# Optimization experiments

Measured on AMD Instinct MI355X. Metric: run time of the kernel, lower is better.

Reference implementation:

```python
import jax, jax.numpy as jnp
import numpy as np

V, E, H, K, B, T = 50000, 256, 256, 32, 64, 512


def _lstm_dir(x, w_ih, w_hh, b, reverse):
    # x: [B,T,D] -> [B,T,H]; torch gate order i,f,g,o; b = b_ih + b_hh combined
    xg = jnp.einsum('btd,gd->btg', x, w_ih) + b          # [B,T,4H]
    xs = jnp.swapaxes(xg, 0, 1)                          # [T,B,4H]
    if reverse:
        xs = xs[::-1]
    Hh = w_hh.shape[1]
    init = (jnp.zeros((x.shape[0], Hh), x.dtype), jnp.zeros((x.shape[0], Hh), x.dtype))

    def step(carry, g_t):
        h, c = carry
        g = g_t + h @ w_hh.T
        i, f, gg, o = jnp.split(g, 4, axis=-1)
        c = jax.nn.sigmoid(f) * c + jax.nn.sigmoid(i) * jnp.tanh(gg)
        h = jax.nn.sigmoid(o) * jnp.tanh(c)
        return (h, c), h

    _, hs = jax.lax.scan(step, init, xs)
    if reverse:
        hs = hs[::-1]
    return jnp.swapaxes(hs, 0, 1)


def _bilstm(x, params):
    out = x
    for (wif, whf, bf, wib, whb, bb) in params:  # inter-layer dropout = identity (eval)
        f = _lstm_dir(out, wif, whf, bf, False)
        bwd = _lstm_dir(out, wib, whb, bb, True)
        out = jnp.concatenate([f, bwd], axis=-1)
    return out


def _crf_loss(em, labels, crf_start, crf_end, crf_trans):
    # numerator (mask is all ones -> every timestep counts)
    num = crf_start[labels[:, 0]] + crf_end[labels[:, -1]]
    num = num + jnp.take_along_axis(em, labels[:, :, None], 2)[..., 0].sum(1)
    num = num + crf_trans[labels[:, :-1], labels[:, 1:]].sum(1)
    # log-partition via forward algorithm
    def pstep(alpha, em_t):
        return jax.nn.logsumexp(alpha[:, :, None] + crf_trans[None], axis=1) + em_t, None

    alpha0 = crf_start[None] + em[:, 0]
    alpha, _ = jax.lax.scan(pstep, alpha0, jnp.swapaxes(em[:, 1:], 0, 1))
    logZ = jax.nn.logsumexp(alpha + crf_end[None], axis=-1)
    # loss = -crf(emissions, labels, mask) with reduction='sum'
    return -(num - logZ).sum()


def _viterbi(em, crf_start, crf_end, crf_trans):
    score0 = crf_start[None] + em[:, 0]

    def vstep(score, em_t):
        ns = score[:, :, None] + crf_trans[None]         # [B,K,K]
        bp = jnp.argmax(ns, axis=1)                      # [B,K]
        return jnp.max(ns, axis=1) + em_t, bp

    score, bps = jax.lax.scan(vstep, score0, jnp.swapaxes(em[:, 1:], 0, 1))
    last = jnp.argmax(score + crf_end[None], axis=-1)    # [B]

    def back(tag, bp):
        prev = jnp.take_along_axis(bp, tag[:, None], axis=1)[:, 0]
        return prev, prev

    _, prevs = jax.lax.scan(back, last, bps[::-1])
    tags = jnp.concatenate([prevs[::-1], last[None]], axis=0)  # [T,B]
    return jnp.swapaxes(tags, 0, 1)


def setup_inputs():
    key = jax.random.key(0)
    ks = iter(jax.random.split(key, 32))
    s = 0.05
    d = {}
    d["input_ids"] = jax.random.randint(next(ks), (B, T), 0, V)
    d["labels"] = jax.random.randint(next(ks), (B, T), 0, K)
    d["mask"] = jnp.ones((B, T), jnp.int32)
    d["emb_table"] = jax.random.normal(next(ks), (V, E)) * s
    for l, din in ((0, E), (1, 2 * H)):
        for dr in ("f", "b"):
            d[f"w_ih_{l}{dr}"] = jax.random.normal(next(ks), (4 * H, din)) * s
            d[f"w_hh_{l}{dr}"] = jax.random.normal(next(ks), (4 * H, H)) * s
            d[f"b_{l}{dr}"] = jax.random.normal(next(ks), (4 * H,)) * s
    d["w_out"] = jax.random.normal(next(ks), (K, 2 * H)) * s
    d["b_out"] = jnp.zeros((K,))
    d["crf_start"] = jax.random.normal(next(ks), (K,)) * s
    d["crf_end"] = jax.random.normal(next(ks), (K,)) * s
    d["crf_trans"] = jax.random.normal(next(ks), (K, K)) * s
    return d


def reference(input_ids, labels, mask, emb_table, w_ih_0f, w_hh_0f, b_0f, w_ih_0b, w_hh_0b, b_0b, w_ih_1f, w_hh_1f, b_1f, w_ih_1b, w_hh_1b, b_1b, w_out, b_out, crf_start, crf_end, crf_trans):
    emb = emb_table[input_ids]  # dropout = identity (eval mode)
    # mask is all ones -> sort/pack/unsort in the original is an identity permutation
    params = [(w_ih_0f, w_hh_0f, b_0f, w_ih_0b, w_hh_0b, b_0b),
              (w_ih_1f, w_hh_1f, b_1f, w_ih_1b, w_hh_1b, b_1b)]
    out = _bilstm(emb, params)                           # [B,T,2H]
    em = jnp.einsum('bth,kh->btk', out, w_out) + b_out   # emissions [B,T,K]
    loss = _crf_loss(em, labels, crf_start, crf_end, crf_trans)
    preds = _viterbi(em, crf_start, crf_end, crf_trans)
    return (loss, preds)
```

## Files before the change

kernel.cpp:

```cpp
#include <hip/hip_runtime.h>
#include <math.h>


constexpr int TLEN = 512, CS = 64, NCH = 8;

constexpr size_t N_OUT  = (size_t)TLEN * 64 * 512;
constexpr size_t O_OUT0 = 0;
constexpr size_t O_OUT1 = N_OUT;
constexpr size_t O_XG   = 2 * N_OUT;
constexpr size_t N_XG   = (size_t)2 * CS * 64 * 1024;
constexpr size_t O_EM   = O_XG;
constexpr size_t O_WQ   = O_XG + N_XG;
constexpr size_t N_WQ   = (size_t)2 * 256 * 256 * 4;
constexpr size_t O_CST  = O_WQ + N_WQ;
constexpr size_t N_CST  = (size_t)2 * 2 * 64 * 256;
constexpr size_t WS_FLOATS = O_CST + N_CST;

__global__ void initz(float* dout) { if (threadIdx.x == 0) dout[0] = 0.f; }

__global__ void ws_too_small_k(float* dout, int n) {
  int i = blockIdx.x * 256 + threadIdx.x;
  if (i < n) dout[i] = 1e30f;
}

__global__ __launch_bounds__(256)
void prep_w(const float* __restrict__ whhf, const float* __restrict__ whhb,
            float* __restrict__ wq) {
  const int k = blockIdx.x & 255, d = blockIdx.x >> 8, u = threadIdx.x;
  const float* W = d ? whhb : whhf;
  float4 v;
  v.x = W[(size_t)(0   + u) * 256 + k];
  v.y = W[(size_t)(256 + u) * 256 + k];
  v.z = W[(size_t)(512 + u) * 256 + k];
  v.w = W[(size_t)(768 + u) * 256 + k];
  reinterpret_cast<float4*>(wq)[(size_t)d * 65536 + k * 256 + u] = v;
}

template <int KTOT, int BN, int MODE>
__global__ __launch_bounds__(256)
void gemm_k(const float* __restrict__ A, const int* __restrict__ ids,
            const float* __restrict__ Wf, const float* __restrict__ Wb,
            const float* __restrict__ bf, const float* __restrict__ bb,
            float* __restrict__ C, int s0) {
  constexpr int BK = 16;
  constexpr int NC = (BN == 128) ? 8 : 2;
  __shared__ float As[BK][132];
  __shared__ float Bs[BK][BN + 4];
  const int tid = threadIdx.x;
  const int m0 = blockIdx.x * 128, n0 = blockIdx.y * BN, d = blockIdx.z;
  const float* W = (MODE < 2 && d) ? Wb : Wf;
  const float* bias = (MODE < 2 && d) ? bb : bf;
  const int mg = tid & 15, ng = tid >> 4;
  const int rb = tid >> 2;
  const int kq = (tid & 3) << 2;

  int arow[2];
  #pragma unroll
  for (int p = 0; p < 2; ++p) {
    if (MODE == 2) {
      arow[p] = m0 + p * 64 + rb;
    } else {
      int s = s0 + (m0 >> 6) + p;
      int t = d ? (TLEN - 1 - s) : s;
      arow[p] = (MODE == 0) ? ids[rb * TLEN + t] : (t * 64 + rb);
    }
  }

  float acc[8][NC];
  #pragma unroll
  for (int i = 0; i < 8; ++i)
    #pragma unroll
    for (int jj = 0; jj < NC; ++jj) acc[i][jj] = 0.f;

  for (int kt = 0; kt < KTOT; kt += BK) {
    #pragma unroll
    for (int p = 0; p < 2; ++p) {
      float4 v = *reinterpret_cast<const float4*>(A + (size_t)arow[p] * KTOT + kt + kq);
      int r = p * 64 + rb;
      As[kq + 0][r] = v.x; As[kq + 1][r] = v.y;
      As[kq + 2][r] = v.z; As[kq + 3][r] = v.w;
    }
    #pragma unroll
    for (int p = 0; p < 2; ++p) {
      int r = p * 64 + rb;
      if (BN == 128 || (p == 0 && rb < BN)) {
        float4 v = *reinterpret_cast<const float4*>(W + (size_t)(n0 + r) * KTOT + kt + kq);
        Bs[kq + 0][r] = v.x; Bs[kq + 1][r] = v.y;
        Bs[kq + 2][r] = v.z; Bs[kq + 3][r] = v.w;
      }
    }
    __syncthreads();
    #pragma unroll
    for (int k = 0; k < BK; ++k) {
      float a[8];
      #pragma unroll
      for (int i = 0; i < 8; ++i) a[i] = As[k][i * 16 + mg];
      if (BN == 128) {
        float w[8];
        float4 w0 = *reinterpret_cast<const float4*>(&Bs[k][ng * 8]);
        float4 w1 = *reinterpret_cast<const float4*>(&Bs[k][ng * 8 + 4]);
        w[0] = w0.x; w[1] = w0.y; w[2] = w0.z; w[3] = w0.w;
        w[4] = w1.x; w[5] = w1.y; w[6] = w1.z; w[7] = w1.w;
        #pragma unroll
        for (int i = 0; i < 8; ++i)
          #pragma unroll
          for (int jj = 0; jj < 8; ++jj) acc[i][jj] += a[i] * w[jj];
      } else {
        float w0 = Bs[k][ng * 2], w1 = Bs[k][ng * 2 + 1];
        #pragma unroll
        for (int i = 0; i < 8; ++i) {
          acc[i][0] += a[i] * w0;
          acc[i][1] += a[i] * w1;
        }
      }
    }
    __syncthreads();
  }

  if (BN == 128) {
    float bv[8];
    #pragma unroll
    for (int jj = 0; jj < 8; ++jj) bv[jj] = bias[n0 + ng * 8 + jj];
    #pragma unroll
    for (int i = 0; i < 8; ++i) {
      const int ml = i * 16 + mg;
      float* cp = C + ((size_t)d * 4096 + m0 + ml) * 1024 + n0 + ng * 8;
      float4 o0, o1;
      o0.x = acc[i][0] + bv[0]; o0.y = acc[i][1] + bv[1];
      o0.z = acc[i][2] + bv[2]; o0.w = acc[i][3] + bv[3];
      o1.x = acc[i][4] + bv[4]; o1.y = acc[i][5] + bv[5];
      o1.z = acc[i][6] + bv[6]; o1.w = acc[i][7] + bv[7];
      reinterpret_cast<float4*>(cp)[0] = o0;
      reinterpret_cast<float4*>(cp)[1] = o1;
    }
  } else {
    const float b0 = bias[ng * 2], b1 = bias[ng * 2 + 1];
    #pragma unroll
    for (int i = 0; i < 8; ++i) {
      const int ml = i * 16 + mg;
      float* cp = C + (size_t)(m0 + ml) * 32 + ng * 2;
      cp[0] = acc[i][0] + b0;
      cp[1] = acc[i][1] + b1;
    }
  }
}

static __device__ __forceinline__ float sigm(float x) { return 1.f / (1.f + expf(-x)); }

__global__ __launch_bounds__(512)
void lstm_bp(const float* __restrict__ xg, const float* __restrict__ wq,
             float* __restrict__ out, float* __restrict__ cst, int s0) {
  const int d = blockIdx.x >> 5;
  const int bp = blockIdx.x & 31;
  const int u = threadIdx.x & 255;
  const int j = threadIdx.x >> 8;
  const int b = bp * 2 + j;
  const float4* wp = reinterpret_cast<const float4*>(wq) + (size_t)d * 65536 + u;
  float* cptr = cst + ((size_t)d * 64 + b) * 256 + u;
  __shared__ float hs[2][2][256];
  float c;
  if (s0 == 0) {
    c = 0.f;
    hs[0][j][u] = 0.f;
  } else {
    c = *cptr;
    const int tp = d ? (TLEN - s0) : (s0 - 1);
    hs[0][j][u] = out[((size_t)tp * 64 + b) * 512 + d * 256 + u];
  }
  __syncthreads();
  int p = 0;
  for (int ls = 0; ls < CS; ++ls) {
    const int s = s0 + ls;
    const int t = d ? (TLEN - 1 - s) : s;
    const size_t xb = (((size_t)d * CS + ls) * 64 + b) * 1024;
    const float xi = xg[xb + u];
    const float xf = xg[xb + 256 + u];
    const float xgv = xg[xb + 512 + u];
    const float xo = xg[xb + 768 + u];
    float ai = 0.f, af = 0.f, ag = 0.f, ao = 0.f;
    const float4* hp = reinterpret_cast<const float4*>(&hs[p][j][0]);
    #pragma unroll 4
    for (int k4 = 0; k4 < 64; ++k4) {
      const float4 h4 = hp[k4];
      const float4 w0 = wp[(k4 * 4 + 0) * 256];
      const float4 w1 = wp[(k4 * 4 + 1) * 256];
      const float4 w2 = wp[(k4 * 4 + 2) * 256];
      const float4 w3 = wp[(k4 * 4 + 3) * 256];
      ai = fmaf(h4.x, w0.x, ai); af = fmaf(h4.x, w0.y, af);
      ag = fmaf(h4.x, w0.z, ag); ao = fmaf(h4.x, w0.w, ao);
      ai = fmaf(h4.y, w1.x, ai); af = fmaf(h4.y, w1.y, af);
      ag = fmaf(h4.y, w1.z, ag); ao = fmaf(h4.y, w1.w, ao);
      ai = fmaf(h4.z, w2.x, ai); af = fmaf(h4.z, w2.y, af);
      ag = fmaf(h4.z, w2.z, ag); ao = fmaf(h4.z, w2.w, ao);
      ai = fmaf(h4.w, w3.x, ai); af = fmaf(h4.w, w3.y, af);
      ag = fmaf(h4.w, w3.z, ag); ao = fmaf(h4.w, w3.w, ao);
    }
    const float gi = sigm(xi + ai), gf = sigm(xf + af);
    const float gc = tanhf(xgv + ag), go = sigm(xo + ao);
    c = gf * c + gi * gc;
    const float h = go * tanhf(c);
    hs[p ^ 1][j][u] = h;
    out[((size_t)t * 64 + b) * 512 + d * 256 + u] = h;
    __syncthreads();
    p ^= 1;
  }
  *cptr = c;
}

__global__ __launch_bounds__(64)
void crf_k(const float* __restrict__ em, const int* __restrict__ labels,
           const float* __restrict__ cs, const float* __restrict__ ce,
           const float* __restrict__ ct, float* __restrict__ dout) {
  __shared__ float trs[32 * 32];
  __shared__ float as_[32];
  __shared__ unsigned char bp[511 * 32];
  const int b = blockIdx.x & 63;
  const bool vit = blockIdx.x >= 64;
  const int lane = threadIdx.x;
  for (int i = lane; i < 1024; i += 64) trs[i] = ct[i];
  __syncthreads();
  const int j = lane & 31, half = lane >> 5, i0 = half * 16;

  if (!vit) {
    float part = 0.f;
    for (int tt = lane; tt < TLEN; tt += 64) {
      int lab = labels[b * TLEN + tt];
      part += em[((size_t)tt * 64 + b) * 32 + lab];
      if (tt) part += trs[labels[b * TLEN + tt - 1] * 32 + lab];
    }
    for (int o = 32; o > 0; o >>= 1) part += __shfl_down(part, o);
    float num = part;
    if (lane == 0) num += cs[labels[b * TLEN]] + ce[labels[b * TLEN + TLEN - 1]];
    if (lane < 32) as_[j] = cs[j] + em[(size_t)b * 32 + j];
    __syncthreads();
    for (int t = 1; t < TLEN; ++t) {
      float m = -1e30f;
      #pragma unroll
      for (int ii = 0; ii < 16; ++ii)
        m = fmaxf(m, as_[i0 + ii] + trs[(i0 + ii) * 32 + j]);
      float s = 0.f;
      #pragma unroll
      for (int ii = 0; ii < 16; ++ii)
        s += expf(as_[i0 + ii] + trs[(i0 + ii) * 32 + j] - m);
      float om = __shfl_xor(m, 32), os = __shfl_xor(s, 32);
      float M = fmaxf(m, om);
      s = s * expf(m - M) + os * expf(om - M);
      float na = M + logf(s) + em[((size_t)t * 64 + b) * 32 + j];
      __syncthreads();
      if (half == 0) as_[j] = na;
      __syncthreads();
    }
    float v = (lane < 32) ? as_[j] + ce[j] : -1e30f;
    float m = v;
    for (int o = 32; o > 0; o >>= 1) m = fmaxf(m, __shfl_xor(m, o));
    float s = (lane < 32) ? expf(v - m) : 0.f;
    for (int o = 32; o > 0; o >>= 1) s += __shfl_xor(s, o);
    if (lane == 0) atomicAdd(dout, -(num - (m + logf(s))));
  } else {
    if (lane < 32) as_[j] = cs[j] + em[(size_t)b * 32 + j];
    __syncthreads();
    for (int t = 1; t < TLEN; ++t) {
      float m = -1e30f; int am = 0;
      #pragma unroll
      for (int ii = 0; ii < 16; ++ii) {
        float v = as_[i0 + ii] + trs[(i0 + ii) * 32 + j];
        if (v > m) { m = v; am = i0 + ii; }
      }
      float om = __shfl_xor(m, 32); int oam = __shfl_xor(am, 32);
      float M; int AM;
      if (half == 0) { if (om > m) { M = om; AM = oam; } else { M = m; AM = am; } }
      else           { if (m > om) { M = m; AM = am; } else { M = om; AM = oam; } }
      float na = M + em[((size_t)t * 64 + b) * 32 + j];
      if (half == 0) bp[(t - 1) * 32 + j] = (unsigned char)AM;
      __syncthreads();
      if (half == 0) as_[j] = na;
      __syncthreads();
    }
    float v = (lane < 32) ? as_[j] + ce[j] : -1e30f;
    int aj = (lane < 32) ? j : 0;
    #pragma unroll
    for (int o = 1; o < 64; o <<= 1) {
      float ov = __shfl_xor(v, o); int oa = __shfl_xor(aj, o);
      if (ov > v || (ov == v && oa < aj)) { v = ov; aj = oa; }
    }
    if (lane == 0) {
      int cur = aj;
      dout[1 + b * TLEN + TLEN - 1] = (float)cur;
      for (int t = TLEN - 1; t >= 1; --t) {
        cur = bp[(t - 1) * 32 + cur];
        dout[1 + b * TLEN + t - 1] = (float)cur;
      }
    }
  }
}

extern "C" void kernel_launch(void* const* d_in, const int* in_sizes, int n_in,
                              void* d_out, int out_size, void* d_ws, size_t ws_size,
                              hipStream_t stream) {
  (void)in_sizes; (void)n_in;
  float* dout = (float*)d_out;
  if (ws_size < WS_FLOATS * sizeof(float)) {
    ws_too_small_k<<<(out_size + 255) / 256, 256, 0, stream>>>(dout, out_size);
    return;
  }
  const int* ids    = (const int*)d_in[0];
  const int* labels = (const int*)d_in[1];
  const float* emb  = (const float*)d_in[3];
  const float* wih0f = (const float*)d_in[4],  *whh0f = (const float*)d_in[5],  *b0f = (const float*)d_in[6];
  const float* wih0b = (const float*)d_in[7],  *whh0b = (const float*)d_in[8],  *b0b = (const float*)d_in[9];
  const float* wih1f = (const float*)d_in[10], *whh1f = (const float*)d_in[11], *b1f = (const float*)d_in[12];
  const float* wih1b = (const float*)d_in[13], *whh1b = (const float*)d_in[14], *b1b = (const float*)d_in[15];
  const float* w_out = (const float*)d_in[16], *b_out = (const float*)d_in[17];
  const float* c_s = (const float*)d_in[18], *c_e = (const float*)d_in[19], *c_t = (const float*)d_in[20];
  float* ws   = (float*)d_ws;
  float* out0 = ws + O_OUT0;
  float* out1 = ws + O_OUT1;
  float* xg   = ws + O_XG;
  float* em   = ws + O_EM;
  float* wq   = ws + O_WQ;
  float* cst  = ws + O_CST;

  initz<<<1, 64, 0, stream>>>(dout);

  prep_w<<<512, 256, 0, stream>>>(whh0f, whh0b, wq);
  for (int k = 0; k < NCH; ++k) {
    gemm_k<256, 128, 0><<<dim3(32, 8, 2), 256, 0, stream>>>(
        emb, ids, wih0f, wih0b, b0f, b0b, xg, k * CS);
    lstm_bp<<<64, 512, 0, stream>>>(xg, wq, out0, cst, k * CS);
  }

  prep_w<<<512, 256, 0, stream>>>(whh1f, whh1b, wq);
  for (int k = 0; k < NCH; ++k) {
    gemm_k<512, 128, 1><<<dim3(32, 8, 2), 256, 0, stream>>>(
        out0, nullptr, wih1f, wih1b, b1f, b1b, xg, k * CS);
    lstm_bp<<<64, 512, 0, stream>>>(xg, wq, out1, cst + 32768, k * CS);
  }

  gemm_k<512, 32, 2><<<dim3(256, 1, 1), 256, 0, stream>>>(
      out1, nullptr, w_out, nullptr, b_out, nullptr, em, 0);
  crf_k<<<128, 64, 0, stream>>>(em, labels, c_s, c_e, c_t, dout);
}
```

Before: 17.01 ms.

## Split K across the two batch halves so each weight load serves both rows

Measured after the change: 21.38 ms. +25.7%, slower.

```diff
diff --git a/kernel.cpp b/kernel.cpp
--- a/kernel.cpp
+++ b/kernel.cpp
@@ -147,7 +147,7 @@
 
 static __device__ __forceinline__ float sigm(float x) { return 1.f / (1.f + expf(-x)); }
 
-__global__ __launch_bounds__(512)
+__global__ __launch_bounds__(512, 2)
 void lstm_bp(const float* __restrict__ xg, const float* __restrict__ wq,
              float* __restrict__ out, float* __restrict__ cst, int s0) {
   const int d = blockIdx.x >> 5;
@@ -155,9 +155,11 @@
   const int u = threadIdx.x & 255;
   const int j = threadIdx.x >> 8;
   const int b = bp * 2 + j;
+  const int kbase = j * 128;
   const float4* wp = reinterpret_cast<const float4*>(wq) + (size_t)d * 65536 + u;
   float* cptr = cst + ((size_t)d * 64 + b) * 256 + u;
   __shared__ float hs[2][2][256];
+  __shared__ float red[4][2][256];
   float c;
   if (s0 == 0) {
     c = 0.f;
@@ -173,28 +175,46 @@
     const int s = s0 + ls;
     const int t = d ? (TLEN - 1 - s) : s;
     const size_t xb = (((size_t)d * CS + ls) * 64 + b) * 1024;
-    const float xi = xg[xb + u];
-    const float xf = xg[xb + 256 + u];
+    const float xi  = xg[xb + u];
+    const float xf  = xg[xb + 256 + u];
     const float xgv = xg[xb + 512 + u];
-    const float xo = xg[xb + 768 + u];
-    float ai = 0.f, af = 0.f, ag = 0.f, ao = 0.f;
-    const float4* hp = reinterpret_cast<const float4*>(&hs[p][j][0]);
-    #pragma unroll 4
-    for (int k4 = 0; k4 < 64; ++k4) {
-      const float4 h4 = hp[k4];
-      const float4 w0 = wp[(k4 * 4 + 0) * 256];
-      const float4 w1 = wp[(k4 * 4 + 1) * 256];
-      const float4 w2 = wp[(k4 * 4 + 2) * 256];
-      const float4 w3 = wp[(k4 * 4 + 3) * 256];
-      ai = fmaf(h4.x, w0.x, ai); af = fmaf(h4.x, w0.y, af);
-      ag = fmaf(h4.x, w0.z, ag); ao = fmaf(h4.x, w0.w, ao);
-      ai = fmaf(h4.y, w1.x, ai); af = fmaf(h4.y, w1.y, af);
-      ag = fmaf(h4.y, w1.z, ag); ao = fmaf(h4.y, w1.w, ao);
-      ai = fmaf(h4.z, w2.x, ai); af = fmaf(h4.z, w2.y, af);
-      ag = fmaf(h4.z, w2.z, ag); ao = fmaf(h4.z, w2.w, ao);
-      ai = fmaf(h4.w, w3.x, ai); af = fmaf(h4.w, w3.y, af);
-      ag = fmaf(h4.w, w3.z, ag); ao = fmaf(h4.w, w3.w, ao);
-    }
+    const float xo  = xg[xb + 768 + u];
+    float p0[4] = {0.f, 0.f, 0.f, 0.f};
+    float p1[4] = {0.f, 0.f, 0.f, 0.f};
+    const float4* h0p = reinterpret_cast<const float4*>(&hs[p][0][kbase]);
+    const float4* h1p = reinterpret_cast<const float4*>(&hs[p][1][kbase]);
+    #pragma unroll
+    for (int kk = 0; kk < 128; kk += 16) {
+      float4 w[16];
+      #pragma unroll
+      for (int i = 0; i < 16; ++i) w[i] = wp[(size_t)(kbase + kk + i) * 256];
+      #pragma unroll
+      for (int q4 = 0; q4 < 4; ++q4) {
+        const float4 h0 = h0p[(kk >> 2) + q4];
+        const float4 h1 = h1p[(kk >> 2) + q4];
+        #pragma unroll
+        for (int q = 0; q < 4; ++q) {
+          const float4 wv = w[q4 * 4 + q];
+          const float e0 = (q == 0) ? h0.x : (q == 1) ? h0.y : (q == 2) ? h0.z : h0.w;
+          const float e1 = (q == 0) ? h1.x : (q == 1) ? h1.y : (q == 2) ? h1.z : h1.w;
+          p0[0] = fmaf(e0, wv.x, p0[0]);
+          p0[1] = fmaf(e0, wv.y, p0[1]);
+          p0[2] = fmaf(e0, wv.z, p0[2]);
+          p0[3] = fmaf(e0, wv.w, p0[3]);
+          p1[0] = fmaf(e1, wv.x, p1[0]);
+          p1[1] = fmaf(e1, wv.y, p1[1]);
+          p1[2] = fmaf(e1, wv.z, p1[2]);
+          p1[3] = fmaf(e1, wv.w, p1[3]);
+        }
+      }
+    }
+    #pragma unroll
+    for (int i = 0; i < 4; ++i) red[i][j][u] = j ? p0[i] : p1[i];
+    __syncthreads();
+    const float ai = (j ? p1[0] : p0[0]) + red[0][j ^ 1][u];
+    const float af = (j ? p1[1] : p0[1]) + red[1][j ^ 1][u];
+    const float ag = (j ? p1[2] : p0[2]) + red[2][j ^ 1][u];
+    const float ao = (j ? p1[3] : p0[3]) + red[3][j ^ 1][u];
     const float gi = sigm(xi + ai), gf = sigm(xf + af);
     const float gc = tanhf(xgv + ag), go = sigm(xo + ao);
     c = gf * c + gi * gc;
```
